# Performance work log

Measured on AMD Instinct MI355X. Metric: run time of the kernel, lower is better.

## Reference

```python
import jax, jax.numpy as jnp
import numpy as np

HID = 2048
HEADS = 16
HEAD_DIM = HID // HEADS  # 128
MLP_HID = 4 * HID
L_IMG = 2048
L_TXT = 256


def _layernorm(x, eps=1e-6):
    mu = jnp.mean(x, axis=-1, keepdims=True)
    xc = x - mu
    var = jnp.mean(xc * xc, axis=-1, keepdims=True)
    return xc * jax.lax.rsqrt(var + eps)


def _rmsnorm(x, scale, eps=1e-6):
    xf = x.astype(jnp.float32)
    rrms = jax.lax.rsqrt(jnp.mean(xf * xf, axis=-1, keepdims=True) + eps)
    return (xf * rrms).astype(x.dtype) * scale


def _apply_rope(x, pe):
    # x: [B,H,L,D], pe: [1,1,L,D/2,2,2]
    B, H, L, D = x.shape
    xf = x.astype(jnp.float32).reshape(B, H, L, D // 2, 1, 2)
    out = pe[..., 0] * xf[..., 0] + pe[..., 1] * xf[..., 1]  # [B,H,L,D/2,2]
    return out.reshape(B, H, L, D).astype(x.dtype)


def _attention(q, k, v, pe):
    q = _apply_rope(q, pe)
    k = _apply_rope(k, pe)
    scale = 1.0 / jnp.sqrt(jnp.float32(q.shape[-1])).astype(q.dtype)
    logits = jnp.einsum('bhqd,bhkd->bhqk', q, k) * scale
    probs = jax.nn.softmax(logits, axis=-1)
    out = jnp.einsum('bhqk,bhkd->bhqd', probs, v)
    B, H, L, D = out.shape
    return out.transpose(0, 2, 1, 3).reshape(B, L, H * D)


def _modulation(vec, w, b):
    out = jnp.dot(jax.nn.silu(vec), w) + b  # [B, 6*dim]
    return jnp.split(out[:, None, :], 6, axis=-1)


def _qkv_heads(x, w, b):
    B, L, _ = x.shape
    qkv = (jnp.dot(x, w) + b).reshape(B, L, 3, HEADS, HEAD_DIM)
    qkv = qkv.transpose(2, 0, 3, 1, 4)  # [3,B,H,L,D]
    return qkv[0], qkv[1], qkv[2]


def _mlp(x, w1, b1, w2, b2):
    return jnp.dot(jax.nn.gelu(jnp.dot(x, w1) + b1, approximate=True), w2) + b2


def setup_inputs() -> dict:
    key = jax.random.key(0)
    ks = iter(jax.random.split(key, 32))
    s = 0.02
    d = {
        'img': jax.random.normal(next(ks), (1, L_IMG, HID), jnp.float32),
        'txt': jax.random.normal(next(ks), (1, L_TXT, HID), jnp.float32),
        'vec': jax.random.normal(next(ks), (1, HID), jnp.float32),
        'pe': jax.random.normal(next(ks), (1, 1, L_TXT + L_IMG, HEAD_DIM // 2, 2, 2), jnp.float32),
    }
    for p in ('img', 'txt'):
        d[p + '_mod_w'] = jax.random.normal(next(ks), (HID, 6 * HID), jnp.float32) * s
        d[p + '_mod_b'] = jnp.zeros((6 * HID,), jnp.float32)
        d[p + '_qkv_w'] = jax.random.normal(next(ks), (HID, 3 * HID), jnp.float32) * s
        d[p + '_qkv_b'] = jnp.zeros((3 * HID,), jnp.float32)
        d[p + '_q_scale'] = jnp.ones((HEAD_DIM,), jnp.float32)
        d[p + '_k_scale'] = jnp.ones((HEAD_DIM,), jnp.float32)
        d[p + '_proj_w'] = jax.random.normal(next(ks), (HID, HID), jnp.float32) * s
        d[p + '_proj_b'] = jnp.zeros((HID,), jnp.float32)
        d[p + '_mlp_w1'] = jax.random.normal(next(ks), (HID, MLP_HID), jnp.float32) * s
        d[p + '_mlp_b1'] = jnp.zeros((MLP_HID,), jnp.float32)
        d[p + '_mlp_w2'] = jax.random.normal(next(ks), (MLP_HID, HID), jnp.float32) * s
        d[p + '_mlp_b2'] = jnp.zeros((HID,), jnp.float32)
    return d


def reference(img, txt, vec, pe,
              img_mod_w, img_mod_b, img_qkv_w, img_qkv_b, img_q_scale, img_k_scale,
              img_proj_w, img_proj_b, img_mlp_w1, img_mlp_b1, img_mlp_w2, img_mlp_b2,
              txt_mod_w, txt_mod_b, txt_qkv_w, txt_qkv_b, txt_q_scale, txt_k_scale,
              txt_proj_w, txt_proj_b, txt_mlp_w1, txt_mlp_b1, txt_mlp_w2, txt_mlp_b2):
    i_sh1, i_sc1, i_g1, i_sh2, i_sc2, i_g2 = _modulation(vec, img_mod_w, img_mod_b)
    t_sh1, t_sc1, t_g1, t_sh2, t_sc2, t_g2 = _modulation(vec, txt_mod_w, txt_mod_b)

    img_modulated = (1 + i_sc1) * _layernorm(img) + i_sh1
    iq, ik, iv = _qkv_heads(img_modulated, img_qkv_w, img_qkv_b)
    iq = _rmsnorm(iq, img_q_scale)
    ik = _rmsnorm(ik, img_k_scale)

    txt_modulated = (1 + t_sc1) * _layernorm(txt) + t_sh1
    tq, tk, tv = _qkv_heads(txt_modulated, txt_qkv_w, txt_qkv_b)
    tq = _rmsnorm(tq, txt_q_scale)
    tk = _rmsnorm(tk, txt_k_scale)

    q = jnp.concatenate((tq, iq), axis=2)
    k = jnp.concatenate((tk, ik), axis=2)
    v = jnp.concatenate((tv, iv), axis=2)
    attn = _attention(q, k, v, pe)  # [B, L_txt+L_img, HID]
    Lt = txt.shape[1]
    txt_attn, img_attn = attn[:, :Lt], attn[:, Lt:]

    img = img + i_g1 * (jnp.dot(img_attn, img_proj_w) + img_proj_b)
    img = img + i_g2 * _mlp((1 + i_sc2) * _layernorm(img) + i_sh2,
                            img_mlp_w1, img_mlp_b1, img_mlp_w2, img_mlp_b2)

    txt = txt + t_g1 * (jnp.dot(txt_attn, txt_proj_w) + txt_proj_b)
    txt = txt + t_g2 * _mlp((1 + t_sc2) * _layernorm(txt) + t_sh2,
                            txt_mlp_w1, txt_mlp_b1, txt_mlp_w2, txt_mlp_b2)
    return img, txt
```

## Files before the change

kernel.cpp:

```cpp
#include <hip/hip_runtime.h>
#include <math.h>

typedef unsigned short u16;
typedef short bf16x8 __attribute__((ext_vector_type(8)));
typedef float f32x4 __attribute__((ext_vector_type(4)));

#define HID 2048
#define NH 16
#define HD 128
#define LI 2048
#define LT 256
#define LA 2304
#define MODW 12288

__device__ __forceinline__ u16 f2bf(float f) {
  unsigned int u = __float_as_uint(f);
  u += 0x7fff + ((u >> 16) & 1);
  return (u16)(u >> 16);
}
__device__ __forceinline__ float bf2f(u16 b) {
  return __uint_as_float(((unsigned int)b) << 16);
}

__device__ __forceinline__ void gload16(const void* g, void* l) {
  __builtin_amdgcn_global_load_lds(
      (const __attribute__((address_space(1))) unsigned int*)g,
      (__attribute__((address_space(3))) unsigned int*)l, 16, 0, 0);
}

__global__ void k_mod_partial(const float* __restrict__ vec,
                              const float* __restrict__ wi,
                              const float* __restrict__ wt,
                              float* __restrict__ part) {
  __shared__ float sv[256];
  int j = blockIdx.x * 256 + threadIdx.x;
  int k0 = blockIdx.y * 256;
  const float* w = blockIdx.z ? wt : wi;
  float v = vec[k0 + threadIdx.x];
  sv[threadIdx.x] = v / (1.f + expf(-v));
  __syncthreads();
  float acc = 0.f;
  for (int kk = 0; kk < 256; ++kk)
    acc += sv[kk] * w[(size_t)(k0 + kk) * MODW + j];
  part[(size_t)(blockIdx.z * 8 + blockIdx.y) * MODW + j] = acc;
}

__global__ void k_mod_reduce(const float* __restrict__ part,
                             const float* __restrict__ bi,
                             const float* __restrict__ bt,
                             float* __restrict__ mod) {
  int i = blockIdx.x * 256 + threadIdx.x;
  int s = i / MODW, j = i % MODW;
  const float* b = s ? bt : bi;
  float v = b[j];
#pragma unroll
  for (int c = 0; c < 8; ++c) v += part[(size_t)(s * 8 + c) * MODW + j];
  mod[i] = v;
}

__global__ void k_ln_mod(const float* __restrict__ xi, const float* __restrict__ xt,
                         const float* __restrict__ shi, const float* __restrict__ sci,
                         const float* __restrict__ sht, const float* __restrict__ sct,
                         u16* __restrict__ out) {
  int r = blockIdx.x;
  bool txs = r < LT;
  const float* xr = txs ? (xt + (size_t)r * HID) : (xi + (size_t)(r - LT) * HID);
  const float* sh = txs ? sht : shi;
  const float* sc = txs ? sct : sci;
  float4 v0 = ((const float4*)xr)[threadIdx.x * 2];
  float4 v1 = ((const float4*)xr)[threadIdx.x * 2 + 1];
  float s1 = v0.x + v0.y + v0.z + v0.w + v1.x + v1.y + v1.z + v1.w;
  float s2 = v0.x * v0.x + v0.y * v0.y + v0.z * v0.z + v0.w * v0.w +
             v1.x * v1.x + v1.y * v1.y + v1.z * v1.z + v1.w * v1.w;
#pragma unroll
  for (int m = 1; m < 64; m <<= 1) { s1 += __shfl_xor(s1, m); s2 += __shfl_xor(s2, m); }
  __shared__ float red[8];
  int wid = threadIdx.x >> 6;
  if ((threadIdx.x & 63) == 0) { red[wid] = s1; red[4 + wid] = s2; }
  __syncthreads();
  float tot  = red[0] + red[1] + red[2] + red[3];
  float tot2 = red[4] + red[5] + red[6] + red[7];
  float mu = tot * (1.f / HID);
  float var = tot2 * (1.f / HID) - mu * mu;
  float rs = rsqrtf(var + 1e-6f);
  int c = threadIdx.x * 8;
  float v[8] = {v0.x, v0.y, v0.z, v0.w, v1.x, v1.y, v1.z, v1.w};
  u16 o[8] __attribute__((aligned(16)));
#pragma unroll
  for (int u = 0; u < 8; ++u)
    o[u] = f2bf((v[u] - mu) * rs * (1.f + sc[c + u]) + sh[c + u]);
  *(uint4*)&out[(size_t)r * HID + c] = *(uint4*)o;
}

__global__ void k_tconv(const float* __restrict__ srcI, const float* __restrict__ srcT,
                        u16* __restrict__ dstI, u16* __restrict__ dstT,
                        int K, int N) {
  __shared__ __align__(16) float t[64][65];
  const float* src = blockIdx.z ? srcT : srcI;
  u16* dst = blockIdx.z ? dstT : dstI;
  int n0 = blockIdx.x * 64, k0 = blockIdx.y * 64;
  int tr = threadIdx.x >> 4;
  int tc = (threadIdx.x & 15) * 4;
#pragma unroll
  for (int i = 0; i < 4; ++i) {
    int r = i * 16 + tr;
    float4 v = *(const float4*)&src[(size_t)(k0 + r) * N + n0 + tc];
    t[r][tc] = v.x; t[r][tc + 1] = v.y; t[r][tc + 2] = v.z; t[r][tc + 3] = v.w;
  }
  __syncthreads();
#pragma unroll
  for (int i = 0; i < 4; ++i) {
    int nr = i * 16 + tr;
    ushort4 o;
    o.x = f2bf(t[tc][nr]); o.y = f2bf(t[tc + 1][nr]);
    o.z = f2bf(t[tc + 2][nr]); o.w = f2bf(t[tc + 3][nr]);
    *(ushort4*)&dst[(size_t)(n0 + nr) * K + k0 + tc] = o;
  }
}

template<int MODE>
__global__ __launch_bounds__(256, 4) void k_gemm(
    const u16* __restrict__ A, int lda,
    const u16* __restrict__ B0, const u16* __restrict__ B1, int ldb,
    void* __restrict__ out0, void* __restrict__ out1, int ldc,
    const float* __restrict__ b0, const float* __restrict__ b1, int K,
    const float* __restrict__ x0, const float* __restrict__ x1,
    const float* __restrict__ g0, const float* __restrict__ g1,
    u16* __restrict__ part) {
  __shared__ __align__(16) u16 lA[128 * 64];
  __shared__ __align__(16) u16 lB[128 * 64];
  int gx = gridDim.x, gy = gridDim.y, nwg = gx * gy;
  int bid = blockIdx.y * gx + blockIdx.x;
  int sw = (bid & 7) * (nwg >> 3) + (bid >> 3);
  int bx = sw / gy, by = sw - bx * gy;
  int m0 = by * 128, n0 = bx * 128;
  bool txs = (m0 < LT);
  const u16* Bt = txs ? B1 : B0;
  const float* bias = txs ? b1 : b0;
  int mr = txs ? m0 : m0 - LT;
  int z = blockIdx.z;
  int Kh = K / (int)gridDim.z;
  int tid = threadIdx.x, lane = tid & 63, wid = tid >> 6;
  int wh = wid >> 1, ww = wid & 1;
  f32x4 acc[4][4] = {};
  const char* Ab = (const char*)(A + (size_t)m0 * lda + (size_t)z * Kh);
  const char* Bb = (const char*)(Bt + (size_t)n0 * ldb + (size_t)z * Kh);
  int ko = (lane >> 4) * 8, cl = lane & 15;
  for (int k0 = 0; k0 < Kh; k0 += 64) {
#pragma unroll
    for (int i = 0; i < 4; ++i) {
      int o = (i * 256 + tid) * 16;
      int r = o >> 7, cb = o & 127;
      gload16(Ab + (size_t)r * (lda * 2) + k0 * 2 + cb, (char*)lA + o);
      gload16(Bb + (size_t)r * (ldb * 2) + k0 * 2 + cb, (char*)lB + o);
    }
    __syncthreads();
#pragma unroll
    for (int kk = 0; kk < 64; kk += 32) {
      bf16x8 a[4], b[4];
#pragma unroll
      for (int m = 0; m < 4; ++m)
        a[m] = *(const bf16x8*)&lA[(wh * 64 + m * 16 + cl) * 64 + kk + ko];
#pragma unroll
      for (int n = 0; n < 4; ++n)
        b[n] = *(const bf16x8*)&lB[(ww * 64 + n * 16 + cl) * 64 + kk + ko];
#pragma unroll
      for (int m = 0; m < 4; ++m)
#pragma unroll
        for (int n = 0; n < 4; ++n)
          acc[m][n] = __builtin_amdgcn_mfma_f32_16x16x32_bf16(a[m], b[n], acc[m][n], 0, 0, 0);
    }
    __syncthreads();
  }
  int rg = (lane >> 4) * 4;
#pragma unroll
  for (int m = 0; m < 4; ++m) {
    int r0 = wh * 64 + m * 16 + rg;
#pragma unroll
    for (int n = 0; n < 4; ++n) {
      int gcol = n0 + ww * 64 + n * 16 + cl;
#pragma unroll
      for (int j = 0; j < 4; ++j) {
        float v = acc[m][n][j];
        if (MODE == 3) {
          part[(size_t)z * (LA * (size_t)HID) + (size_t)(m0 + r0 + j) * ldc + gcol] = f2bf(v);
        } else {
          v += bias[gcol];
          size_t orow = (size_t)(mr + r0 + j);
          if (MODE == 0) {
            ((float*)(txs ? out1 : out0))[orow * ldc + gcol] = v;
          } else if (MODE == 4) {
            ((u16*)(txs ? out1 : out0))[orow * ldc + gcol] = f2bf(v);
          } else if (MODE == 1) {
            float z2 = 1.5957691216057308f * (v + 0.044715f * v * v * v);
            ((u16*)(txs ? out1 : out0))[orow * ldc + gcol] =
                f2bf(v / (1.f + __expf(-z2)));
          } else {
            const float* xin = txs ? x1 : x0;
            const float* g = txs ? g1 : g0;
            ((float*)(txs ? out1 : out0))[orow * ldc + gcol] =
                xin[orow * ldc + gcol] + g[gcol] * v;
          }
        }
      }
    }
  }
}

template<int NZ>
__global__ void k_red(const u16* __restrict__ P,
                      const float* __restrict__ bias0, const float* __restrict__ bias1,
                      const float* __restrict__ g0, const float* __restrict__ g1,
                      const float* __restrict__ xi, const float* __restrict__ xt,
                      float* __restrict__ oimg, float* __restrict__ otxt) {
  size_t i = ((size_t)blockIdx.x * 256 + threadIdx.x) * 4;
  const size_t S = (size_t)LA * HID;
  int row = (int)(i >> 11), col = (int)(i & (HID - 1));
  float s0 = 0.f, s1 = 0.f, s2 = 0.f, s3 = 0.f;
#pragma unroll
  for (int z = 0; z < NZ; ++z) {
    ushort4 a = *(const ushort4*)&P[i + (size_t)z * S];
    s0 += bf2f(a.x); s1 += bf2f(a.y); s2 += bf2f(a.z); s3 += bf2f(a.w);
  }
  bool txs = row < LT;
  const float* bias = txs ? bias1 : bias0;
  const float* g = txs ? g1 : g0;
  size_t off = txs ? (size_t)row * HID + col : (size_t)(row - LT) * HID + col;
  const float* xin = (txs ? xt : xi) + off;
  float* out = (txs ? otxt : oimg) + off;
  float4 x = *(const float4*)xin;
  float4 o;
  o.x = x.x + g[col] * (s0 + bias[col]);
  o.y = x.y + g[col + 1] * (s1 + bias[col + 1]);
  o.z = x.z + g[col + 2] * (s2 + bias[col + 2]);
  o.w = x.w + g[col + 3] * (s3 + bias[col + 3]);
  *(float4*)out = o;
}

__global__ void k_qkv_post(const u16* __restrict__ qkv,
                           const float* __restrict__ qsi, const float* __restrict__ ksi,
                           const float* __restrict__ qst, const float* __restrict__ kst,
                           const float* __restrict__ pe,
                           u16* __restrict__ Q, u16* __restrict__ K, u16* __restrict__ V) {
  int h = blockIdx.x, lg = blockIdx.y, lane = threadIdx.x;
  bool txs = lg < LT;
  const float* qs = txs ? qst : qsi;
  const float* ks = txs ? kst : ksi;
  const u16* base = qkv + (size_t)lg * 6144 + h * HD;
  float q0 = bf2f(base[2 * lane]), q1 = bf2f(base[2 * lane + 1]);
  float k0 = bf2f(base[2048 + 2 * lane]), k1 = bf2f(base[2048 + 2 * lane + 1]);
  float v0 = bf2f(base[4096 + 2 * lane]), v1 = bf2f(base[4096 + 2 * lane + 1]);
  float sq = q0 * q0 + q1 * q1, sk = k0 * k0 + k1 * k1;
#pragma unroll
  for (int m = 1; m < 64; m <<= 1) { sq += __shfl_xor(sq, m); sk += __shfl_xor(sk, m); }
  float rq = rsqrtf(sq * (1.f / HD) + 1e-6f), rk = rsqrtf(sk * (1.f / HD) + 1e-6f);
  q0 *= rq * qs[2 * lane]; q1 *= rq * qs[2 * lane + 1];
  k0 *= rk * ks[2 * lane]; k1 *= rk * ks[2 * lane + 1];
  float4 p = *(const float4*)&pe[(size_t)lg * 256 + lane * 4];
  float qa = p.x * q0 + p.y * q1, qb = p.z * q0 + p.w * q1;
  float ka = p.x * k0 + p.y * k1, kb = p.z * k0 + p.w * k1;
  size_t ob = ((size_t)h * LA + lg) * HD + 2 * lane;
  Q[ob] = f2bf(qa); Q[ob + 1] = f2bf(qb);
  K[ob] = f2bf(ka); K[ob + 1] = f2bf(kb);
  V[ob] = f2bf(v0); V[ob + 1] = f2bf(v1);
}

__global__ void k_vtrans(const u16* __restrict__ V, u16* __restrict__ Vt) {
  __shared__ __align__(16) u16 t[64][72];
  int l0 = blockIdx.x * 64, d0 = blockIdx.y * 64, h = blockIdx.z;
  const u16* src = V + (size_t)h * LA * HD;
#pragma unroll
  for (int jj = 0; jj < 2; ++jj) {
    int idx = (jj * 256 + threadIdx.x) * 8;
    int r = idx >> 6, c = idx & 63;
    *(uint4*)&t[r][c] = *(const uint4*)&src[(size_t)(l0 + r) * HD + d0 + c];
  }
  __syncthreads();
  u16* dst = Vt + (size_t)h * HD * LA;
#pragma unroll
  for (int jj = 0; jj < 2; ++jj) {
    int idx = (jj * 256 + threadIdx.x) * 8;
    int r = idx >> 6, c = idx & 63;
    u16 o[8] __attribute__((aligned(16)));
#pragma unroll
    for (int u = 0; u < 8; ++u) o[u] = t[c + u][r];
    *(uint4*)&dst[(size_t)(d0 + r) * LA + l0 + c] = *(uint4*)o;
  }
}

__global__ __launch_bounds__(576) void k_flash(
    const u16* __restrict__ Q, const u16* __restrict__ Kg,
    const u16* __restrict__ Vt, u16* __restrict__ attn) {
  __shared__ __align__(16) u16 Ks[2][64 * 128];
  __shared__ __align__(16) u16 Vs[2][128 * 64];
  __shared__ __align__(16) u16 Ps[9][16 * 64];
  int bid = blockIdx.y * gridDim.x + blockIdx.x;
  int xcd = bid & 7, j0 = bid >> 3;
  int h = xcd * 2 + (j0 >> 4);
  int q0 = (j0 & 15) * 144;
  int tid = threadIdx.x, lane = tid & 63, w = tid >> 6;
  int ko = (lane >> 4) * 8, cl = lane & 15;
  const char* Kb = (const char*)(Kg + (size_t)h * LA * HD);
  const char* Vb = (const char*)(Vt + (size_t)h * HD * LA);
  bf16x8 qf[4];
  {
    const u16* Qr = Q + ((size_t)h * LA + q0 + w * 16 + cl) * HD;
#pragma unroll
    for (int kk = 0; kk < 4; ++kk) qf[kk] = *(const bf16x8*)&Qr[kk * 32 + ko];
  }
  f32x4 oacc[8] = {};
  float mst[4] = {-1e30f, -1e30f, -1e30f, -1e30f};
  float lst[4] = {0.f, 0.f, 0.f, 0.f};

  auto stage = [&](int t0, int buf) {
    if (tid < 512) {
#pragma unroll
      for (int i = 0; i < 2; ++i) {
        int o = (i * 512 + tid) * 16;
        int r = o >> 8, c = o & 255;
        gload16(Kb + (size_t)(t0 + r) * 256 + (c ^ ((r & 7) << 4)),
                (char*)Ks[buf] + o);
        int r2 = o >> 7, c2 = o & 127;
        gload16(Vb + (size_t)r2 * (LA * 2) + (size_t)t0 * 2 + (c2 ^ ((r2 & 7) << 4)),
                (char*)Vs[buf] + o);
      }
    }
  };

  stage(0, 0);
  __syncthreads();
  for (int t = 0; t < LA / 64; ++t) {
    int buf = t & 1;
    if (t < LA / 64 - 1) stage((t + 1) * 64, buf ^ 1);
    f32x4 sacc[4] = {};
    __builtin_amdgcn_s_setprio(1);
#pragma unroll
    for (int kk = 0; kk < 4; ++kk) {
      int cb = (kk * 32 + ko) * 2;
#pragma unroll
      for (int n = 0; n < 4; ++n) {
        int row = n * 16 + cl;
        bf16x8 bk = *(const bf16x8*)&Ks[buf][row * 128 + ((cb ^ ((row & 7) << 4)) >> 1)];
        sacc[n] = __builtin_amdgcn_mfma_f32_16x16x32_bf16(qf[kk], bk, sacc[n], 0, 0, 0);
      }
    }
    __builtin_amdgcn_s_setprio(0);
    const float scale = 0.08838834764831845f;
    float mx[4];
#pragma unroll
    for (int j = 0; j < 4; ++j) {
      float m1 = -1e30f;
#pragma unroll
      for (int n = 0; n < 4; ++n) { sacc[n][j] *= scale; m1 = fmaxf(m1, sacc[n][j]); }
#pragma unroll
      for (int m = 1; m < 16; m <<= 1) m1 = fmaxf(m1, __shfl_xor(m1, m));
      mx[j] = m1;
    }
    float dmax = fmaxf(fmaxf(mx[0] - mst[0], mx[1] - mst[1]),
                       fmaxf(mx[2] - mst[2], mx[3] - mst[3]));
    if (!__all(dmax <= 8.f)) {
#pragma unroll
      for (int j = 0; j < 4; ++j) {
        float mnew = fmaxf(mst[j], mx[j]);
        float alpha = __expf(mst[j] - mnew);
        lst[j] *= alpha; mst[j] = mnew;
#pragma unroll
        for (int nd = 0; nd < 8; ++nd) oacc[nd][j] *= alpha;
      }
    }
    float p[4][4];
#pragma unroll
    for (int j = 0; j < 4; ++j) {
      float s = 0.f;
#pragma unroll
      for (int n = 0; n < 4; ++n) { p[n][j] = __expf(sacc[n][j] - mst[j]); s += p[n][j]; }
#pragma unroll
      for (int m = 1; m < 16; m <<= 1) s += __shfl_xor(s, m);
      lst[j] += s;
    }
#pragma unroll
    for (int j = 0; j < 4; ++j) {
      int pr = (lane >> 4) * 4 + j;
#pragma unroll
      for (int n = 0; n < 4; ++n)
        Ps[w][pr * 64 + ((((n * 16 + cl) * 2) ^ ((pr & 7) << 4)) >> 1)] = f2bf(p[n][j]);
    }
    __builtin_amdgcn_s_setprio(1);
#pragma unroll
    for (int kk = 0; kk < 64; kk += 32) {
      int cb = (kk + ko) * 2;
      bf16x8 ap = *(const bf16x8*)&Ps[w][cl * 64 + ((cb ^ ((cl & 7) << 4)) >> 1)];
#pragma unroll
      for (int nd = 0; nd < 8; ++nd) {
        int vr = nd * 16 + cl;
        bf16x8 bv = *(const bf16x8*)&Vs[buf][vr * 64 + ((cb ^ ((vr & 7) << 4)) >> 1)];
        oacc[nd] = __builtin_amdgcn_mfma_f32_16x16x32_bf16(ap, bv, oacc[nd], 0, 0, 0);
      }
    }
    __builtin_amdgcn_s_setprio(0);
    __syncthreads();
  }
#pragma unroll
  for (int j = 0; j < 4; ++j) {
    int lrow = q0 + w * 16 + (lane >> 4) * 4 + j;
    float inv = 1.f / lst[j];
#pragma unroll
    for (int nd = 0; nd < 8; ++nd)
      attn[(size_t)lrow * HID + h * HD + nd * 16 + cl] = f2bf(oacc[nd][j] * inv);
  }
}

extern "C" void kernel_launch(void* const* d_in, const int* in_sizes, int n_in,
                              void* d_out, int out_size, void* d_ws, size_t ws_size,
                              hipStream_t stream) {
  const float* img = (const float*)d_in[0];
  const float* txt = (const float*)d_in[1];
  const float* vec = (const float*)d_in[2];
  const float* pe  = (const float*)d_in[3];
  const float* imod_w = (const float*)d_in[4];
  const float* imod_b = (const float*)d_in[5];
  const float* iqkv_w = (const float*)d_in[6];
  const float* iqkv_b = (const float*)d_in[7];
  const float* iq_s   = (const float*)d_in[8];
  const float* ik_s   = (const float*)d_in[9];
  const float* iproj_w = (const float*)d_in[10];
  const float* iproj_b = (const float*)d_in[11];
  const float* imlp_w1 = (const float*)d_in[12];
  const float* imlp_b1 = (const float*)d_in[13];
  const float* imlp_w2 = (const float*)d_in[14];
  const float* imlp_b2 = (const float*)d_in[15];
  const float* tmod_w = (const float*)d_in[16];
  const float* tmod_b = (const float*)d_in[17];
  const float* tqkv_w = (const float*)d_in[18];
  const float* tqkv_b = (const float*)d_in[19];
  const float* tq_s   = (const float*)d_in[20];
  const float* tk_s   = (const float*)d_in[21];
  const float* tproj_w = (const float*)d_in[22];
  const float* tproj_b = (const float*)d_in[23];
  const float* tmlp_w1 = (const float*)d_in[24];
  const float* tmlp_b1 = (const float*)d_in[25];
  const float* tmlp_w2 = (const float*)d_in[26];
  const float* tmlp_b2 = (const float*)d_in[27];
  (void)in_sizes; (void)n_in; (void)out_size; (void)ws_size;

  float* oimg = (float*)d_out;
  float* otxt = oimg + (size_t)LI * HID;

  char* p = (char*)d_ws;
  auto alloc = [&](size_t b) { char* r = p; p += (b + 255) & ~(size_t)255; return r; };
  float* part = (float*)alloc((size_t)16 * MODW * 4);
  float* mod  = (float*)alloc((size_t)2 * MODW * 4);
  u16*  xm    = (u16*)alloc((size_t)LA * HID * 2);
  u16*  wt_i  = (u16*)alloc((size_t)8192 * 2048 * 2);
  u16*  wt_t  = (u16*)alloc((size_t)8192 * 2048 * 2);
  u16*  qkvr  = (u16*)alloc((size_t)LA * 6144 * 2);
  u16*  Qb    = (u16*)alloc((size_t)NH * LA * HD * 2);
  u16*  Kb    = (u16*)alloc((size_t)NH * LA * HD * 2);
  u16*  Vb    = (u16*)alloc((size_t)NH * LA * HD * 2);
  u16*  Vtb   = (u16*)alloc((size_t)NH * LA * HD * 2);
  u16*  attn  = (u16*)alloc((size_t)LA * HID * 2);
  u16*  hb    = (u16*)alloc((size_t)LA * 8192 * 2);
  u16*  kpart = (u16*)alloc((size_t)4 * LA * HID * 2);

  const float* MI = mod;
  const float* MT = mod + MODW;

  k_mod_partial<<<dim3(48, 8, 2), 256, 0, stream>>>(vec, imod_w, tmod_w, part);
  k_mod_reduce<<<dim3(96), 256, 0, stream>>>(part, imod_b, tmod_b, mod);

  k_ln_mod<<<dim3(LA), 256, 0, stream>>>(img, txt, MI, MI + 2048, MT, MT + 2048, xm);

  k_tconv<<<dim3(96, 32, 2), 256, 0, stream>>>(iqkv_w, tqkv_w, wt_i, wt_t, 2048, 6144);
  k_gemm<4><<<dim3(48, 18), 256, 0, stream>>>(xm, 2048, wt_i, wt_t, 2048,
      qkvr + (size_t)LT * 6144, qkvr, 6144, iqkv_b, tqkv_b, 2048,
      nullptr, nullptr, nullptr, nullptr, nullptr);

  k_qkv_post<<<dim3(NH, LA), 64, 0, stream>>>(qkvr, iq_s, ik_s, tq_s, tk_s, pe, Qb, Kb, Vb);
  k_vtrans<<<dim3(36, 2, NH), 256, 0, stream>>>(Vb, Vtb);

  k_flash<<<dim3(16, NH), 576, 0, stream>>>(Qb, Kb, Vtb, attn);

  k_tconv<<<dim3(32, 32, 2), 256, 0, stream>>>(iproj_w, tproj_w, wt_i, wt_t, 2048, 2048);
  k_gemm<2><<<dim3(16, 18), 256, 0, stream>>>(attn, 2048, wt_i, wt_t, 2048,
      oimg, otxt, 2048, iproj_b, tproj_b, 2048,
      img, txt, MI + 4096, MT + 4096, nullptr);

  k_ln_mod<<<dim3(LA), 256, 0, stream>>>(oimg, otxt, MI + 6144, MI + 8192,
                                         MT + 6144, MT + 8192, xm);

  k_tconv<<<dim3(128, 32, 2), 256, 0, stream>>>(imlp_w1, tmlp_w1, wt_i, wt_t, 2048, 8192);
  k_gemm<1><<<dim3(64, 18), 256, 0, stream>>>(xm, 2048, wt_i, wt_t, 2048,
      hb + (size_t)LT * 8192, hb, 8192, imlp_b1, tmlp_b1, 2048,
      nullptr, nullptr, nullptr, nullptr, nullptr);

  k_tconv<<<dim3(32, 128, 2), 256, 0, stream>>>(imlp_w2, tmlp_w2, wt_i, wt_t, 8192, 2048);
  k_gemm<3><<<dim3(16, 18, 4), 256, 0, stream>>>(hb, 8192, wt_i, wt_t, 8192,
      nullptr, nullptr, 2048, nullptr, nullptr, 8192,
      nullptr, nullptr, nullptr, nullptr, kpart);
  k_red<4><<<dim3(4608), 256, 0, stream>>>(kpart, imlp_b2, tmlp_b2,
      MI + 10240, MT + 10240, oimg, otxt, oimg, otxt);
}
```

Before: 652.6 us.

## Fuse fp32 weight transpose and bf16 conversion into GEMM B-tile loading

```diff
diff --git a/kernel.cpp b/kernel.cpp
--- a/kernel.cpp
+++ b/kernel.cpp
@@ -92,36 +92,10 @@
   *(uint4*)&out[(size_t)r * HID + c] = *(uint4*)o;
 }
 
-__global__ void k_tconv(const float* __restrict__ srcI, const float* __restrict__ srcT,
-                        u16* __restrict__ dstI, u16* __restrict__ dstT,
-                        int K, int N) {
-  __shared__ __align__(16) float t[64][65];
-  const float* src = blockIdx.z ? srcT : srcI;
-  u16* dst = blockIdx.z ? dstT : dstI;
-  int n0 = blockIdx.x * 64, k0 = blockIdx.y * 64;
-  int tr = threadIdx.x >> 4;
-  int tc = (threadIdx.x & 15) * 4;
-#pragma unroll
-  for (int i = 0; i < 4; ++i) {
-    int r = i * 16 + tr;
-    float4 v = *(const float4*)&src[(size_t)(k0 + r) * N + n0 + tc];
-    t[r][tc] = v.x; t[r][tc + 1] = v.y; t[r][tc + 2] = v.z; t[r][tc + 3] = v.w;
-  }
-  __syncthreads();
-#pragma unroll
-  for (int i = 0; i < 4; ++i) {
-    int nr = i * 16 + tr;
-    ushort4 o;
-    o.x = f2bf(t[tc][nr]); o.y = f2bf(t[tc + 1][nr]);
-    o.z = f2bf(t[tc + 2][nr]); o.w = f2bf(t[tc + 3][nr]);
-    *(ushort4*)&dst[(size_t)(n0 + nr) * K + k0 + tc] = o;
-  }
-}
-
 template<int MODE>
 __global__ __launch_bounds__(256, 4) void k_gemm(
     const u16* __restrict__ A, int lda,
-    const u16* __restrict__ B0, const u16* __restrict__ B1, int ldb,
+    const float* __restrict__ B0, const float* __restrict__ B1, int ldbN,
     void* __restrict__ out0, void* __restrict__ out1, int ldc,
     const float* __restrict__ b0, const float* __restrict__ b1, int K,
     const float* __restrict__ x0, const float* __restrict__ x1,
@@ -135,7 +109,7 @@
   int bx = sw / gy, by = sw - bx * gy;
   int m0 = by * 128, n0 = bx * 128;
   bool txs = (m0 < LT);
-  const u16* Bt = txs ? B1 : B0;
+  const float* Bf = txs ? B1 : B0;
   const float* bias = txs ? b1 : b0;
   int mr = txs ? m0 : m0 - LT;
   int z = blockIdx.z;
@@ -144,15 +118,32 @@
   int wh = wid >> 1, ww = wid & 1;
   f32x4 acc[4][4] = {};
   const char* Ab = (const char*)(A + (size_t)m0 * lda + (size_t)z * Kh);
-  const char* Bb = (const char*)(Bt + (size_t)n0 * ldb + (size_t)z * Kh);
+  const float* Bb = Bf + (size_t)z * Kh * ldbN + n0;
   int ko = (lane >> 4) * 8, cl = lane & 15;
+  int tn = (tid & 31) * 4;
+  int tk = (tid >> 5) * 8;
   for (int k0 = 0; k0 < Kh; k0 += 64) {
 #pragma unroll
     for (int i = 0; i < 4; ++i) {
       int o = (i * 256 + tid) * 16;
       int r = o >> 7, cb = o & 127;
       gload16(Ab + (size_t)r * (lda * 2) + k0 * 2 + cb, (char*)lA + o);
-      gload16(Bb + (size_t)r * (ldb * 2) + k0 * 2 + cb, (char*)lB + o);
+    }
+    {
+      const float* src = Bb + (size_t)(k0 + tk) * ldbN + tn;
+      float4 L[8];
+#pragma unroll
+      for (int kk = 0; kk < 8; ++kk)
+        L[kk] = *(const float4*)(src + (size_t)kk * ldbN);
+#pragma unroll
+      for (int j = 0; j < 4; ++j) {
+        int row = tn + j;
+        u16 pk[8] __attribute__((aligned(16)));
+#pragma unroll
+        for (int kk = 0; kk < 8; ++kk) pk[kk] = f2bf(((const float*)&L[kk])[j]);
+        int s = ((row ^ (row >> 2)) & 7) << 4;
+        *(uint4*)((char*)lB + row * 128 + ((tk * 2) ^ s)) = *(uint4*)pk;
+      }
     }
     __syncthreads();
 #pragma unroll
@@ -162,8 +153,11 @@
       for (int m = 0; m < 4; ++m)
         a[m] = *(const bf16x8*)&lA[(wh * 64 + m * 16 + cl) * 64 + kk + ko];
 #pragma unroll
-      for (int n = 0; n < 4; ++n)
-        b[n] = *(const bf16x8*)&lB[(ww * 64 + n * 16 + cl) * 64 + kk + ko];
+      for (int n = 0; n < 4; ++n) {
+        int row = ww * 64 + n * 16 + cl;
+        int s = ((row ^ (row >> 2)) & 7) << 4;
+        b[n] = *(const bf16x8*)((const char*)lB + row * 128 + (((kk + ko) * 2) ^ s));
+      }
 #pragma unroll
       for (int m = 0; m < 4; ++m)
 #pragma unroll
@@ -451,8 +445,6 @@
   float* part = (float*)alloc((size_t)16 * MODW * 4);
   float* mod  = (float*)alloc((size_t)2 * MODW * 4);
   u16*  xm    = (u16*)alloc((size_t)LA * HID * 2);
-  u16*  wt_i  = (u16*)alloc((size_t)8192 * 2048 * 2);
-  u16*  wt_t  = (u16*)alloc((size_t)8192 * 2048 * 2);
   u16*  qkvr  = (u16*)alloc((size_t)LA * 6144 * 2);
   u16*  Qb    = (u16*)alloc((size_t)NH * LA * HD * 2);
   u16*  Kb    = (u16*)alloc((size_t)NH * LA * HD * 2);
@@ -470,8 +462,7 @@
 
   k_ln_mod<<<dim3(LA), 256, 0, stream>>>(img, txt, MI, MI + 2048, MT, MT + 2048, xm);
 
-  k_tconv<<<dim3(96, 32, 2), 256, 0, stream>>>(iqkv_w, tqkv_w, wt_i, wt_t, 2048, 6144);
-  k_gemm<4><<<dim3(48, 18), 256, 0, stream>>>(xm, 2048, wt_i, wt_t, 2048,
+  k_gemm<4><<<dim3(48, 18), 256, 0, stream>>>(xm, 2048, iqkv_w, tqkv_w, 6144,
       qkvr + (size_t)LT * 6144, qkvr, 6144, iqkv_b, tqkv_b, 2048,
       nullptr, nullptr, nullptr, nullptr, nullptr);
 
@@ -480,21 +471,18 @@
 
   k_flash<<<dim3(16, NH), 576, 0, stream>>>(Qb, Kb, Vtb, attn);
 
-  k_tconv<<<dim3(32, 32, 2), 256, 0, stream>>>(iproj_w, tproj_w, wt_i, wt_t, 2048, 2048);
-  k_gemm<2><<<dim3(16, 18), 256, 0, stream>>>(attn, 2048, wt_i, wt_t, 2048,
+  k_gemm<2><<<dim3(16, 18), 256, 0, stream>>>(attn, 2048, iproj_w, tproj_w, 2048,
       oimg, otxt, 2048, iproj_b, tproj_b, 2048,
       img, txt, MI + 4096, MT + 4096, nullptr);
 
   k_ln_mod<<<dim3(LA), 256, 0, stream>>>(oimg, otxt, MI + 6144, MI + 8192,
                                          MT + 6144, MT + 8192, xm);
 
-  k_tconv<<<dim3(128, 32, 2), 256, 0, stream>>>(imlp_w1, tmlp_w1, wt_i, wt_t, 2048, 8192);
-  k_gemm<1><<<dim3(64, 18), 256, 0, stream>>>(xm, 2048, wt_i, wt_t, 2048,
+  k_gemm<1><<<dim3(64, 18), 256, 0, stream>>>(xm, 2048, imlp_w1, tmlp_w1, 8192,
       hb + (size_t)LT * 8192, hb, 8192, imlp_b1, tmlp_b1, 2048,
       nullptr, nullptr, nullptr, nullptr, nullptr);
 
-  k_tconv<<<dim3(32, 128, 2), 256, 0, stream>>>(imlp_w2, tmlp_w2, wt_i, wt_t, 8192, 2048);
-  k_gemm<3><<<dim3(16, 18, 4), 256, 0, stream>>>(hb, 8192, wt_i, wt_t, 8192,
+  k_gemm<3><<<dim3(16, 18, 4), 256, 0, stream>>>(hb, 8192, imlp_w2, tmlp_w2, 2048,
       nullptr, nullptr, 2048, nullptr, nullptr, 8192,
       nullptr, nullptr, nullptr, nullptr, kpart);
   k_red<4><<<dim3(4608), 256, 0, stream>>>(kpart, imlp_b2, tmlp_b2,
```

Result: slower. 839.8 us (+28.7%).
